# Optimization experiments

Measured on AMD Instinct MI355X. Metric: run time of the kernel, lower is better.

The kernel has to match this reference:

```python
import jax, jax.numpy as jnp
import numpy as np

N_NODES = 100000
N_EDGES = 800000
NUM_RADIAL = 6
HIDDEN = 128
VOCAB = 95


def swish(v):
    return v * jax.nn.sigmoid(v)


def setup_inputs() -> dict:
    key = jax.random.key(0)
    ks = jax.random.split(key, 10)
    x = jax.random.randint(ks[0], (N_NODES,), 0, VOCAB, dtype=jnp.int64 if jax.config.jax_enable_x64 else jnp.int32)
    chi = jax.random.normal(ks[1], (N_NODES, HIDDEN), dtype=jnp.float32)
    rbf = jax.random.normal(ks[2], (N_EDGES, NUM_RADIAL), dtype=jnp.float32)
    i = jax.random.randint(ks[3], (N_EDGES,), 0, N_NODES)
    j = jax.random.randint(ks[4], (N_EDGES,), 0, N_NODES)
    emb_table = jax.random.normal(ks[5], (VOCAB, HIDDEN), dtype=jnp.float32) * (1.0 / np.sqrt(HIDDEN))
    W_rbf = jax.random.normal(ks[6], (NUM_RADIAL, HIDDEN), dtype=jnp.float32) * (1.0 / np.sqrt(NUM_RADIAL))
    b_rbf = jnp.zeros((HIDDEN,), dtype=jnp.float32)
    W = jax.random.normal(ks[7], (5 * HIDDEN, HIDDEN), dtype=jnp.float32) * (1.0 / np.sqrt(5 * HIDDEN))
    b = jnp.zeros((HIDDEN,), dtype=jnp.float32)
    return {"x": x, "chi": chi, "rbf": rbf, "i": i, "j": j,
            "emb_table": emb_table, "W_rbf": W_rbf, "b_rbf": b_rbf, "W": W, "b": b}


def reference(x, chi, rbf, i, j, emb_table, W_rbf, b_rbf, W, b):
    # node embedding lookup: [N, H]
    x_emb = emb_table[x]
    # rbf0 = swish(Linear(rbf)): [E, H]
    rbf0 = swish(rbf @ W_rbf + b_rbf)
    # lin over concat([x[i], chi[i], x[j], chi[j], rbf0]) split into 5 chunks of W
    # to avoid materializing the [E, 5H] concat tensor.
    H = emb_table.shape[1]
    W1, W2, W3, W4, W5 = (W[0 * H:1 * H], W[1 * H:2 * H], W[2 * H:3 * H],
                          W[3 * H:4 * H], W[4 * H:5 * H])
    pre = (x_emb[i] @ W1 + chi[i] @ W2 + x_emb[j] @ W3 + chi[j] @ W4
           + rbf0 @ W5 + b)
    e = swish(pre)
    return (e, 1)
```

## Files before the change

### kernel.cpp

```cpp
#include <hip/hip_runtime.h>
#include <hip/hip_bf16.h>

#define HIDDEN 128
#define NRAD 6

typedef short bf16x8 __attribute__((ext_vector_type(8)));
typedef float f32x4 __attribute__((ext_vector_type(4)));

__device__ __forceinline__ float swishf(float z) {
    return z / (1.0f + __expf(-z));
}

__device__ __forceinline__ unsigned short f2bf(float f) {
    unsigned int u = __float_as_uint(f);
    unsigned int r = (u + 0x7FFFu + ((u >> 16) & 1u)) >> 16;
    return (unsigned short)r;
}

__device__ __forceinline__ float bf2f(unsigned int s) {
    return __uint_as_float(s << 16);
}

__device__ __forceinline__ unsigned int pk2bf(float x, float y) {
    __hip_bfloat162 h = __float22bfloat162_rn(make_float2(x, y));
    return *reinterpret_cast<unsigned int*>(&h);
}

__device__ __forceinline__ f32x4 fmav(float s, f32x4 w, f32x4 z) {
    z[0] += s * w[0]; z[1] += s * w[1]; z[2] += s * w[2]; z[3] += s * w[3];
    return z;
}

__global__ void k_emb_proj(const float* __restrict__ emb, const float* __restrict__ W,
                           const float* __restrict__ bvec,
                           float* __restrict__ T1, float* __restrict__ T3,
                           float* __restrict__ out_scalar) {
    int v = blockIdx.x;
    int h = threadIdx.x;
    if (v == 0 && h == 0) *out_scalar = 1.0f;
    const float* er = emb + v * HIDDEN;
    float a1 = bvec[h], a3 = 0.f;
    #pragma unroll 4
    for (int k = 0; k < HIDDEN; ++k) {
        float e = er[k];
        a1 += e * W[k * HIDDEN + h];
        a3 += e * W[(256 + k) * HIDDEN + h];
    }
    T1[v * HIDDEN + h] = a1;
    T3[v * HIDDEN + h] = a3;
}

__global__ void k_wprep(const float* __restrict__ W, short* __restrict__ wf) {
    int gid = blockIdx.x * 256 + threadIdx.x;
    int m = gid >> 11;
    int t = gid & 2047;
    int l = t & 63;
    int tile = t >> 6;
    int n = tile >> 2, kt = tile & 3;
    int k0 = kt * 32 + (l >> 4) * 8;
    int col = n * 16 + (l & 15);
    static const int rowoff[3] = {128, 384, 512};
    const float* Wm = W + rowoff[m] * HIDDEN;
    bf16x8 v;
    #pragma unroll
    for (int j = 0; j < 8; ++j) v[j] = (short)f2bf(Wm[(k0 + j) * HIDDEN + col]);
    *(bf16x8*)(wf + (size_t)gid * 8) = v;
}

#define NB 64
__global__ __launch_bounds__(256) void k_node(const int* __restrict__ x,
        const float* __restrict__ chi,
        const short* __restrict__ w2f, const short* __restrict__ w4f,
        const float* __restrict__ T1, const float* __restrict__ T3,
        short* __restrict__ Abf, short* __restrict__ Bbf, int n_nodes) {
    __shared__ unsigned short chi_s[NB * HIDDEN];
    __shared__ int x_s[NB];
    int n0 = blockIdx.x * NB;
    int t = threadIdx.x;
    int l = t & 63;
    int wv = t >> 6;

    #pragma unroll
    for (int it = 0; it < 8; ++it) {
        int q = t + it * 256;
        int row = q >> 5, s = q & 31;
        int gn = n0 + row;
        float4 c = (gn < n_nodes) ? *(const float4*)(chi + (size_t)gn * HIDDEN + s * 4)
                                  : make_float4(0.f, 0.f, 0.f, 0.f);
        unsigned int lo = pk2bf(c.x, c.y), hi = pk2bf(c.z, c.w);
        unsigned int byte = (unsigned int)(row * 256 + s * 8) ^ ((row & 7) << 4);
        *(uint2*)((char*)chi_s + byte) = make_uint2(lo, hi);
    }
    if (t < NB) {
        int gn = n0 + t;
        x_s[t] = (gn < n_nodes) ? x[gn] : 0;
    }
    __syncthreads();

    bf16x8 cfrag[4];
    {
        int rloc = wv * 16 + (l & 15);
        unsigned int base = (unsigned int)(rloc * 256 + (l >> 4) * 16);
        unsigned int swz = (unsigned int)((rloc & 7) << 4);
        #pragma unroll
        for (int kt = 0; kt < 4; ++kt)
            cfrag[kt] = *(const bf16x8*)((const char*)chi_s + ((base + kt * 64) ^ swz));
    }

    int nd_loc = wv * 16 + (l & 15);
    int gn = n0 + nd_loc;
    int xv = x_s[nd_loc];
    int g = l >> 4;
    int hq = g * 4;
    bool live = (gn < n_nodes);
    short* arow = Abf + (size_t)gn * HIDDEN + g * 32;
    short* brow = Bbf + (size_t)gn * HIDDEN + g * 32;

    #pragma unroll
    for (int np = 0; np < 4; ++np) {
        uint4 oa, ob;
        #pragma unroll
        for (int half = 0; half < 2; ++half) {
            int n = 2 * np + half;
            f32x4 aA = {0.f, 0.f, 0.f, 0.f};
            f32x4 aB = {0.f, 0.f, 0.f, 0.f};
            #pragma unroll
            for (int kt = 0; kt < 4; ++kt) {
                bf16x8 w2 = *(const bf16x8*)(w2f + ((size_t)(n * 4 + kt) * 64 + l) * 8);
                bf16x8 w4 = *(const bf16x8*)(w4f + ((size_t)(n * 4 + kt) * 64 + l) * 8);
                aA = __builtin_amdgcn_mfma_f32_16x16x32_bf16(w2, cfrag[kt], aA, 0, 0, 0);
                aB = __builtin_amdgcn_mfma_f32_16x16x32_bf16(w4, cfrag[kt], aB, 0, 0, 0);
            }
            if (live) {
                int h = n * 16 + hq;
                float4 t1 = *(const float4*)(T1 + (size_t)xv * HIDDEN + h);
                float4 t3 = *(const float4*)(T3 + (size_t)xv * HIDDEN + h);
                unsigned int a0 = pk2bf(aA[0] + t1.x, aA[1] + t1.y);
                unsigned int a1 = pk2bf(aA[2] + t1.z, aA[3] + t1.w);
                unsigned int b0 = pk2bf(aB[0] + t3.x, aB[1] + t3.y);
                unsigned int b1 = pk2bf(aB[2] + t3.z, aB[3] + t3.w);
                if (half == 0) { oa.x = a0; oa.y = a1; ob.x = b0; ob.y = b1; }
                else           { oa.z = a0; oa.w = a1; ob.z = b0; ob.w = b1; }
            }
        }
        if (live) {
            *(uint4*)(arow + np * 8) = oa;
            *(uint4*)(brow + np * 8) = ob;
        }
    }
}

#define EB 64
__global__ __launch_bounds__(256) void k_edge(const float* __restrict__ rbf,
        const int* __restrict__ ei, const int* __restrict__ ej,
        const float* __restrict__ W_rbf, const float* __restrict__ b_rbf,
        const short* __restrict__ w5f,
        const short* __restrict__ Abf, const short* __restrict__ Bbf,
        float* __restrict__ out, int n_edges) {
    __shared__ uint4 smem4[39424 / 16];
    char* base = (char*)smem4;
    short* w5_s  = (short*)base;
    float* wrb_s = (float*)(base + 33792);
    float* rbf_sf = (float*)(base + 37376);
    int*   i_s   = (int*)(base + 38912);
    int*   j_s   = (int*)(base + 39168);

    int e0 = blockIdx.x * EB;
    int t = threadIdx.x;
    int l = t & 63;
    int wv = t >> 6;
    int g = l >> 4;
    int er = l & 15;

    #pragma unroll
    for (int it = 0; it < 8; ++it) {
        int q = t + it * 256;
        ((uint4*)w5_s)[q] = ((const uint4*)w5f)[q];
    }
    for (int q = t; q < 7 * HIDDEN; q += 256)
        wrb_s[q] = (q < 6 * HIDDEN) ? W_rbf[q] : b_rbf[q - 6 * HIDDEN];
    for (int q = t; q < EB * NRAD + 2 * EB; q += 256) {
        if (q < EB * NRAD) {
            int gidx = e0 * NRAD + q;
            rbf_sf[q] = (gidx < n_edges * NRAD) ? rbf[gidx] : 0.f;
        } else if (q < EB * NRAD + EB) {
            int e = q - EB * NRAD;
            int ge = e0 + e;
            i_s[e] = (ge < n_edges) ? ei[ge] : 0;
        } else {
            int e = q - EB * NRAD - EB;
            int ge = e0 + e;
            j_s[e] = (ge < n_edges) ? ej[ge] : 0;
        }
    }
    __syncthreads();

    int e_loc = wv * 16 + er;
    const short* ap = Abf + (size_t)i_s[e_loc] * HIDDEN + g * 32;
    const short* bp = Bbf + (size_t)j_s[e_loc] * HIDDEN + g * 32;
    uint4 avq[4], bvq[4];
    #pragma unroll
    for (int q = 0; q < 4; ++q) {
        avq[q] = *(const uint4*)(ap + q * 8);
        bvq[q] = *(const uint4*)(bp + q * 8);
    }

    float rb[NRAD];
    #pragma unroll
    for (int r = 0; r < NRAD; ++r) rb[r] = rbf_sf[e_loc * NRAD + r];

    bf16x8 pfrag[4];
    #pragma unroll
    for (int kt = 0; kt < 4; ++kt) {
        int cb = kt * 32 + g * 8;
        f32x4 z0 = *(const f32x4*)(wrb_s + 6 * HIDDEN + cb);
        f32x4 z1 = *(const f32x4*)(wrb_s + 6 * HIDDEN + cb + 4);
        #pragma unroll
        for (int r = 0; r < NRAD; ++r) {
            z0 = fmav(rb[r], *(const f32x4*)(wrb_s + r * HIDDEN + cb), z0);
            z1 = fmav(rb[r], *(const f32x4*)(wrb_s + r * HIDDEN + cb + 4), z1);
        }
        union { bf16x8 v; unsigned int u[4]; } pu;
        pu.u[0] = pk2bf(swishf(z0[0]), swishf(z0[1]));
        pu.u[1] = pk2bf(swishf(z0[2]), swishf(z0[3]));
        pu.u[2] = pk2bf(swishf(z1[0]), swishf(z1[1]));
        pu.u[3] = pk2bf(swishf(z1[2]), swishf(z1[3]));
        pfrag[kt] = pu.v;
    }

    f32x4 acc[8];
    #pragma unroll
    for (int n = 0; n < 8; ++n) {
        f32x4 a = {0.f, 0.f, 0.f, 0.f};
        #pragma unroll
        for (int kt = 0; kt < 4; ++kt) {
            bf16x8 wfr = *(const bf16x8*)(w5_s + ((n * 4 + kt) * 64 + l) * 8);
            a = __builtin_amdgcn_mfma_f32_16x16x32_bf16(wfr, pfrag[kt], a, 0, 0, 0);
        }
        acc[n] = a;
    }
    __syncthreads();

    bool full = (e0 + EB <= n_edges);
    char* seg = base + wv * 8448;

    if (full) {
        #pragma unroll
        for (int n = 0; n < 8; ++n) {
            unsigned int au0 = (n & 1) ? avq[n >> 1].z : avq[n >> 1].x;
            unsigned int au1 = (n & 1) ? avq[n >> 1].w : avq[n >> 1].y;
            unsigned int bu0 = (n & 1) ? bvq[n >> 1].z : bvq[n >> 1].x;
            unsigned int bu1 = (n & 1) ? bvq[n >> 1].w : bvq[n >> 1].y;
            f32x4 o;
            o[0] = swishf(acc[n][0] + bf2f(au0 & 0xffffu) + bf2f(bu0 & 0xffffu));
            o[1] = swishf(acc[n][1] + bf2f(au0 >> 16) + bf2f(bu0 >> 16));
            o[2] = swishf(acc[n][2] + bf2f(au1 & 0xffffu) + bf2f(bu1 & 0xffffu));
            o[3] = swishf(acc[n][3] + bf2f(au1 >> 16) + bf2f(bu1 >> 16));
            *(f32x4*)(seg + er * 528 + n * 64 + g * 16) = o;
        }
        #pragma unroll
        for (int li = 0; li < 4; ++li) {
            #pragma unroll
            for (int eh = 0; eh < 2; ++eh) {
                int e = eh * 8 + (l >> 3);
                int s = l & 7;
                f32x4 v = *(const f32x4*)(seg + e * 528 + li * 128 + s * 16);
                float* dst = out + (size_t)(e0 + wv * 16 + e) * HIDDEN + li * 32 + s * 4;
                __builtin_nontemporal_store(v, (f32x4*)dst);
            }
        }
    } else {
        int ge = e0 + e_loc;
        #pragma unroll
        for (int n = 0; n < 8; ++n) {
            if (ge < n_edges) {
                unsigned int au0 = (n & 1) ? avq[n >> 1].z : avq[n >> 1].x;
                unsigned int au1 = (n & 1) ? avq[n >> 1].w : avq[n >> 1].y;
                unsigned int bu0 = (n & 1) ? bvq[n >> 1].z : bvq[n >> 1].x;
                unsigned int bu1 = (n & 1) ? bvq[n >> 1].w : bvq[n >> 1].y;
                f32x4 o;
                o[0] = swishf(acc[n][0] + bf2f(au0 & 0xffffu) + bf2f(bu0 & 0xffffu));
                o[1] = swishf(acc[n][1] + bf2f(au0 >> 16) + bf2f(bu0 >> 16));
                o[2] = swishf(acc[n][2] + bf2f(au1 & 0xffffu) + bf2f(bu1 & 0xffffu));
                o[3] = swishf(acc[n][3] + bf2f(au1 >> 16) + bf2f(bu1 >> 16));
                *(f32x4*)(out + (size_t)ge * HIDDEN + n * 16 + g * 4) = o;
            }
        }
    }
}

extern "C" void kernel_launch(void* const* d_in, const int* in_sizes, int n_in,
                              void* d_out, int out_size, void* d_ws, size_t ws_size,
                              hipStream_t stream) {
    const int*   x     = (const int*)d_in[0];
    const float* chi   = (const float*)d_in[1];
    const float* rbf   = (const float*)d_in[2];
    const int*   ei    = (const int*)d_in[3];
    const int*   ej    = (const int*)d_in[4];
    const float* emb   = (const float*)d_in[5];
    const float* W_rbf = (const float*)d_in[6];
    const float* b_rbf = (const float*)d_in[7];
    const float* W     = (const float*)d_in[8];
    const float* bvec  = (const float*)d_in[9];
    float* out = (float*)d_out;

    int n_nodes = in_sizes[0];
    int n_edges = in_sizes[3];
    int vocab   = in_sizes[5] / HIDDEN;

    short* Abf = (short*)d_ws;
    short* Bbf = Abf + (size_t)n_nodes * HIDDEN;
    float* T1  = (float*)(Bbf + (size_t)n_nodes * HIDDEN);
    float* T3  = T1 + (size_t)vocab * HIDDEN;
    short* wf  = (short*)(T3 + (size_t)vocab * HIDDEN);
    short* w2f = wf;
    short* w4f = wf + 16384;
    short* w5f = wf + 32768;

    k_emb_proj<<<vocab, HIDDEN, 0, stream>>>(emb, W, bvec, T1, T3, out + (out_size - 1));
    k_wprep<<<24, 256, 0, stream>>>(W, wf);
    k_node<<<(n_nodes + NB - 1) / NB, 256, 0, stream>>>(x, chi, w2f, w4f, T1, T3,
                                                        Abf, Bbf, n_nodes);
    k_edge<<<(n_edges + EB - 1) / EB, 256, 0, stream>>>(rbf, ei, ej, W_rbf, b_rbf,
                                                        w5f, Abf, Bbf, out, n_edges);
}
```

Before: 229.5 us.

## Compute rbf projection with MFMA and permute W5 fragments to match output layout

```diff
diff --git a/kernel.cpp b/kernel.cpp
--- a/kernel.cpp
+++ b/kernel.cpp
@@ -24,11 +24,6 @@
 __device__ __forceinline__ unsigned int pk2bf(float x, float y) {
     __hip_bfloat162 h = __float22bfloat162_rn(make_float2(x, y));
     return *reinterpret_cast<unsigned int*>(&h);
-}
-
-__device__ __forceinline__ f32x4 fmav(float s, f32x4 w, f32x4 z) {
-    z[0] += s * w[0]; z[1] += s * w[1]; z[2] += s * w[2]; z[3] += s * w[3];
-    return z;
 }
 
 __global__ void k_emb_proj(const float* __restrict__ emb, const float* __restrict__ W,
@@ -50,21 +45,51 @@
     T3[v * HIDDEN + h] = a3;
 }
 
-__global__ void k_wprep(const float* __restrict__ W, short* __restrict__ wf) {
+__global__ void k_wprep(const float* __restrict__ W,
+                        const float* __restrict__ W_rbf, const float* __restrict__ b_rbf,
+                        short* __restrict__ wf, short* __restrict__ wrbf) {
     int gid = blockIdx.x * 256 + threadIdx.x;
-    int m = gid >> 11;
-    int t = gid & 2047;
-    int l = t & 63;
-    int tile = t >> 6;
-    int n = tile >> 2, kt = tile & 3;
-    int k0 = kt * 32 + (l >> 4) * 8;
-    int col = n * 16 + (l & 15);
-    static const int rowoff[3] = {128, 384, 512};
-    const float* Wm = W + rowoff[m] * HIDDEN;
-    bf16x8 v;
-    #pragma unroll
-    for (int j = 0; j < 8; ++j) v[j] = (short)f2bf(Wm[(k0 + j) * HIDDEN + col]);
-    *(bf16x8*)(wf + (size_t)gid * 8) = v;
+    if (gid < 4096) {
+        int m = gid >> 11;
+        int t = gid & 2047;
+        int l = t & 63;
+        int tile = t >> 6;
+        int n = tile >> 2, kt = tile & 3;
+        int k0 = kt * 32 + (l >> 4) * 8;
+        int col = n * 16 + (l & 15);
+        const float* Wm = W + (m == 0 ? 128 : 384) * HIDDEN;
+        bf16x8 v;
+        #pragma unroll
+        for (int j = 0; j < 8; ++j) v[j] = (short)f2bf(Wm[(k0 + j) * HIDDEN + col]);
+        *(bf16x8*)(wf + (size_t)gid * 8) = v;
+    } else if (gid < 6144) {
+        int t = gid - 4096;
+        int l = t & 63;
+        int tile = t >> 6;
+        int n = tile >> 2, kt = tile & 3;
+        int g = l >> 4;
+        int col = n * 16 + (l & 15);
+        const float* W5 = W + 512 * HIDDEN;
+        bf16x8 v;
+        #pragma unroll
+        for (int j = 0; j < 8; ++j) {
+            int hk = 32 * kt + 16 * (j >> 2) + 4 * g + (j & 3);
+            v[j] = (short)f2bf(W5[hk * HIDDEN + col]);
+        }
+        *(bf16x8*)(wf + (size_t)gid * 8) = v;
+    } else if (gid < 6272) {
+        int t2 = gid - 6144;
+        int n = t2 >> 4, e = t2 & 15;
+        int hp = n * 16 + e;
+        bf16x8 v;
+        #pragma unroll
+        for (int j = 0; j < 8; ++j) {
+            float val = (j < NRAD) ? W_rbf[j * HIDDEN + hp]
+                      : (j == 6 ? b_rbf[hp] : 0.f);
+            v[j] = (short)f2bf(val);
+        }
+        *(bf16x8*)(wrbf + (size_t)t2 * 8) = v;
+    }
 }
 
 #define NB 64
@@ -153,17 +178,16 @@
 #define EB 64
 __global__ __launch_bounds__(256) void k_edge(const float* __restrict__ rbf,
         const int* __restrict__ ei, const int* __restrict__ ej,
-        const float* __restrict__ W_rbf, const float* __restrict__ b_rbf,
-        const short* __restrict__ w5f,
+        const short* __restrict__ w5f, const short* __restrict__ wrbf,
         const short* __restrict__ Abf, const short* __restrict__ Bbf,
         float* __restrict__ out, int n_edges) {
-    __shared__ uint4 smem4[39424 / 16];
+    __shared__ uint4 smem4[36096 / 16];
     char* base = (char*)smem4;
-    short* w5_s  = (short*)base;
-    float* wrb_s = (float*)(base + 33792);
-    float* rbf_sf = (float*)(base + 37376);
-    int*   i_s   = (int*)(base + 38912);
-    int*   j_s   = (int*)(base + 39168);
+    short* w5_s   = (short*)base;
+    short* wrbf_s = (short*)(base + 32768);
+    unsigned short* rbf_b = (unsigned short*)(base + 34816);
+    int*   i_s    = (int*)(base + 35584);
+    int*   j_s    = (int*)(base + 35840);
 
     int e0 = blockIdx.x * EB;
     int t = threadIdx.x;
@@ -177,12 +201,13 @@
         int q = t + it * 256;
         ((uint4*)w5_s)[q] = ((const uint4*)w5f)[q];
     }
-    for (int q = t; q < 7 * HIDDEN; q += 256)
-        wrb_s[q] = (q < 6 * HIDDEN) ? W_rbf[q] : b_rbf[q - 6 * HIDDEN];
-    for (int q = t; q < EB * NRAD + 2 * EB; q += 256) {
+    if (t < 128) ((uint4*)wrbf_s)[t] = ((const uint4*)wrbf)[t];
+    #pragma unroll
+    for (int it = 0; it < 2; ++it) {
+        int q = t + it * 256;
         if (q < EB * NRAD) {
             int gidx = e0 * NRAD + q;
-            rbf_sf[q] = (gidx < n_edges * NRAD) ? rbf[gidx] : 0.f;
+            rbf_b[q] = (gidx < n_edges * NRAD) ? f2bf(rbf[gidx]) : (unsigned short)0;
         } else if (q < EB * NRAD + EB) {
             int e = q - EB * NRAD;
             int ge = e0 + e;
@@ -205,26 +230,41 @@
         bvq[q] = *(const uint4*)(bp + q * 8);
     }
 
-    float rb[NRAD];
-    #pragma unroll
-    for (int r = 0; r < NRAD; ++r) rb[r] = rbf_sf[e_loc * NRAD + r];
-
+    union { bf16x8 v; unsigned int u[4]; } rbfrag;
+    {
+        const char* rp = (const char*)rbf_b + e_loc * 12;
+        unsigned int q0 = *(const unsigned int*)(rp);
+        unsigned int q1 = *(const unsigned int*)(rp + 4);
+        unsigned int q2 = *(const unsigned int*)(rp + 8);
+        bool g0 = (g == 0);
+        rbfrag.u[0] = g0 ? q0 : 0u;
+        rbfrag.u[1] = g0 ? q1 : 0u;
+        rbfrag.u[2] = g0 ? q2 : 0u;
+        rbfrag.u[3] = g0 ? 0x00003F80u : 0u;
+    }
+    f32x4 accp[8];
+    #pragma unroll
+    for (int n = 0; n < 8; ++n) {
+        bf16x8 wa = *(const bf16x8*)(wrbf_s + (n * 16 + er) * 8);
+        f32x4 z = {0.f, 0.f, 0.f, 0.f};
+        accp[n] = __builtin_amdgcn_mfma_f32_16x16x32_bf16(wa, rbfrag.v, z, 0, 0, 0);
+    }
+    unsigned int word0[8], word1[8];
+    #pragma unroll
+    for (int n = 0; n < 8; ++n) {
+        float s0 = swishf(accp[n][0]), s1 = swishf(accp[n][1]);
+        float s2 = swishf(accp[n][2]), s3 = swishf(accp[n][3]);
+        word0[n] = pk2bf(s0, s1);
+        word1[n] = pk2bf(s2, s3);
+    }
     bf16x8 pfrag[4];
     #pragma unroll
     for (int kt = 0; kt < 4; ++kt) {
-        int cb = kt * 32 + g * 8;
-        f32x4 z0 = *(const f32x4*)(wrb_s + 6 * HIDDEN + cb);
-        f32x4 z1 = *(const f32x4*)(wrb_s + 6 * HIDDEN + cb + 4);
-        #pragma unroll
-        for (int r = 0; r < NRAD; ++r) {
-            z0 = fmav(rb[r], *(const f32x4*)(wrb_s + r * HIDDEN + cb), z0);
-            z1 = fmav(rb[r], *(const f32x4*)(wrb_s + r * HIDDEN + cb + 4), z1);
-        }
         union { bf16x8 v; unsigned int u[4]; } pu;
-        pu.u[0] = pk2bf(swishf(z0[0]), swishf(z0[1]));
-        pu.u[1] = pk2bf(swishf(z0[2]), swishf(z0[3]));
-        pu.u[2] = pk2bf(swishf(z1[0]), swishf(z1[1]));
-        pu.u[3] = pk2bf(swishf(z1[2]), swishf(z1[3]));
+        pu.u[0] = word0[2 * kt];
+        pu.u[1] = word1[2 * kt];
+        pu.u[2] = word0[2 * kt + 1];
+        pu.u[3] = word1[2 * kt + 1];
         pfrag[kt] = pu.v;
     }
 
@@ -316,11 +356,12 @@
     short* w2f = wf;
     short* w4f = wf + 16384;
     short* w5f = wf + 32768;
+    short* wrbf = wf + 49152;
 
     k_emb_proj<<<vocab, HIDDEN, 0, stream>>>(emb, W, bvec, T1, T3, out + (out_size - 1));
-    k_wprep<<<24, 256, 0, stream>>>(W, wf);
+    k_wprep<<<25, 256, 0, stream>>>(W, W_rbf, b_rbf, wf, wrbf);
     k_node<<<(n_nodes + NB - 1) / NB, 256, 0, stream>>>(x, chi, w2f, w4f, T1, T3,
                                                         Abf, Bbf, n_nodes);
-    k_edge<<<(n_edges + EB - 1) / EB, 256, 0, stream>>>(rbf, ei, ej, W_rbf, b_rbf,
-                                                        w5f, Abf, Bbf, out, n_edges);
-}
+    k_edge<<<(n_edges + EB - 1) / EB, 256, 0, stream>>>(rbf, ei, ej, w5f, wrbf,
+                                                        Abf, Bbf, out, n_edges);
+}
```

New measurement: 210.4 us. 1.09x faster.
